# Kernel optimization log

Hardware: AMD Instinct MI355X
Metric: run time of the kernel (lower is better)

The kernel has to match this reference:

```python
import jax, jax.numpy as jnp
import numpy as np

THETA = 1.0
DILATIONS = (1, 2, 3, 4)
EPS = 1e-6


def _scale_features(x, d):
    # x: [B, C, H, W]; one pyramid scale (dilation d)
    B, C, H, W = x.shape
    k = 3 + 2 * (d - 1)          # kernel size per original formula
    pad = d * d                   # pad so effective span d*(k-1)+1 = 2d^2+1 preserves HxW
    K = k * k
    patches = jax.lax.conv_general_dilated_patches(
        x, (k, k), (1, 1), [(pad, pad), (pad, pad)], rhs_dilation=(d, d)
    )  # [B, C*K, H, W], channel-major per input channel
    p = patches.reshape(B, C, K, H, W)

    mu = p.mean(axis=2, keepdims=True)
    diff = p - mu
    var_biased = (diff * diff).mean(axis=2)                 # E[(p-mu)^2]
    std = jnp.sqrt(var_biased * (K / (K - 1))) + EPS        # torch .std is unbiased (ddof=1)

    contrast = var_biased / (std * std)                     # mean(normed^2)
    energy = (p * p).mean(axis=2)
    entropy = -(p * jnp.log(p + EPS)).mean(axis=2)
    # NB: original precedence -> 1.0 / mean(1 + |p - mu|)
    homogeneity = 1.0 / ((1.0 + jnp.abs(diff)).mean(axis=2))

    feats = jnp.stack([contrast, energy, entropy, homogeneity], axis=2)  # [B, C, 4, H, W]
    # martingale transform: exp(theta*log(f+eps) - 0.5*theta^2)
    M = jnp.exp(THETA * jnp.log(feats + EPS) - 0.5 * THETA ** 2)
    return M.reshape(B, C * 4, H, W)  # cat over channels of per-channel feature stacks


def setup_inputs() -> dict:
    key = jax.random.key(0)
    x = jax.random.uniform(key, (2, 4, 256, 256), dtype=jnp.float32)
    return {"x": x}


def reference(x):
    return tuple(_scale_features(x, d) for d in DILATIONS)
```

## Files before the change

### kernel.cpp

```cpp
#include <hip/hip_runtime.h>
#include <cstddef>

#define EPS 1e-6f
constexpr float INV_SQRT_E = 0.6065306597126334f;

template <int D>
__device__ __forceinline__ void body(const float* __restrict__ x,
                                     float* __restrict__ out,
                                     char* smem, int bc, int H, int W)
{
    constexpr int PAD = D * D;
    constexpr int KS  = 2 * D + 1;
    constexpr int K   = KS * KS;
    constexpr int TW  = 64, TH = 8;
    constexpr int LW  = TW + 2 * PAD;
    constexpr int LH  = TH + 2 * PAD;
    constexpr int NE  = LH * LW;
    constexpr int NI2 = (NE + 1023) / 1024;
    constexpr float INVK = 1.0f / (float)K;
    constexpr float UNB  = (float)K / (float)(K - 1);

    float*  sx  = (float*)smem;
    float*  slg = sx + NE;
    float2* cs2 = (float2*)(slg + NE);
    float*  cs1 = (float*)(cs2 + TH * LW);
    float*  muP  = (float*)cs2;
    float*  sadP = muP + TH * 64;

    const int w0 = blockIdx.x * TW;
    const int h0 = blockIdx.y * TH;
    const float* xp = x + (size_t)bc * H * W;
    const int tid = threadIdx.y * 64 + threadIdx.x;

    float v0b[NI2], v1b[NI2];
    #pragma unroll
    for (int i = 0; i < NI2; ++i) {
        const int e0 = 2 * (tid + i * 512);
        float v0 = 0.0f, v1 = 0.0f;
        if (e0 < NE) {
            const int r  = e0 / LW;
            const int cc = e0 - r * LW;
            const int gh = h0 - PAD + r;
            const int gw = w0 - PAD + cc;
            if (gh >= 0 && gh < H) {
                if constexpr ((PAD & 1) == 0) {
                    if (gw >= 0 && gw + 1 < W) {
                        const float2 v = *(const float2*)&xp[gh * W + gw];
                        v0 = v.x; v1 = v.y;
                    } else {
                        if (gw >= 0 && gw < W)         v0 = xp[gh * W + gw];
                        if (gw + 1 >= 0 && gw + 1 < W) v1 = xp[gh * W + gw + 1];
                    }
                } else {
                    if (gw >= 0 && gw < W)         v0 = xp[gh * W + gw];
                    if (gw + 1 >= 0 && gw + 1 < W) v1 = xp[gh * W + gw + 1];
                }
            }
        }
        v0b[i] = v0; v1b[i] = v1;
    }
    #pragma unroll
    for (int i = 0; i < NI2; ++i) {
        const int e0 = 2 * (tid + i * 512);
        if (e0 < NE) {
            *(float2*)&sx[e0]  = make_float2(v0b[i], v1b[i]);
            *(float2*)&slg[e0] = make_float2(v0b[i] * __logf(v0b[i] + EPS),
                                             v1b[i] * __logf(v1b[i] + EPS));
        }
    }
    __syncthreads();

    const int tx = threadIdx.x;
    const int ty = threadIdx.y;

    if constexpr (K <= 9) {
        const float* bx = sx  + ty * LW + tx;
        const float* bl = slg + ty * LW + tx;
        float s = 0.f, s2 = 0.f, sl = 0.f, ta[K];
        #pragma unroll
        for (int mi = 0; mi < KS; ++mi)
            #pragma unroll
            for (int mj = 0; mj < KS; ++mj) {
                const float v = bx[mi * LW + mj];
                ta[mi * KS + mj] = v;
                s  += v;
                s2  = fmaf(v, v, s2);
                sl += bl[mi * LW + mj];
            }
        const float mu = s * INVK;
        float sad = 0.f;
        #pragma unroll
        for (int i = 0; i < K; ++i) sad += fabsf(ta[i] - mu);

        const float energy   = s2 * INVK;
        const float var      = fmaxf(energy - mu * mu, 0.f);
        const float sd       = __builtin_amdgcn_sqrtf(var * UNB) + EPS;
        const float contrast = var * __builtin_amdgcn_rcpf(sd * sd);
        const float entropy  = -sl * INVK;
        const float homog    = __builtin_amdgcn_rcpf(fmaf(sad, INVK, 1.0f));
        const size_t fs = (size_t)H * W;
        const size_t ro = (size_t)(h0 + ty) * W;
        float* op = out + (size_t)bc * 4 * fs + w0 + tx;
        __builtin_nontemporal_store((contrast + EPS) * INV_SQRT_E, &op[0 * fs + ro]);
        __builtin_nontemporal_store((energy   + EPS) * INV_SQRT_E, &op[1 * fs + ro]);
        __builtin_nontemporal_store((entropy  + EPS) * INV_SQRT_E, &op[2 * fs + ro]);
        __builtin_nontemporal_store((homog    + EPS) * INV_SQRT_E, &op[3 * fs + ro]);
        return;
    } else {
        constexpr int HW2 = LW / 2;
        if (tid < 4 * HW2) {
            const int p  = tid / HW2;
            const int c2 = (tid - p * HW2) * 2;
            if (!(D == 3 && p == 3)) {
                const int vA = (D == 2) ? ((p < 2) ? p : p + 2) : p;
                const int vB = vA + D;
                const float2* cx = (const float2*)(sx + vA * LW + c2);
                float sA0=0,sA1=0,qA0=0,qA1=0,sB0=0,sB1=0,qB0=0,qB1=0;
                #pragma unroll
                for (int t = 0; t <= KS; ++t) {
                    const float2 v = cx[t * D * HW2];
                    if (t < KS) { sA0 += v.x; sA1 += v.y;
                                  qA0 = fmaf(v.x,v.x,qA0); qA1 = fmaf(v.y,v.y,qA1); }
                    if (t >= 1) { sB0 += v.x; sB1 += v.y;
                                  qB0 = fmaf(v.x,v.x,qB0); qB1 = fmaf(v.y,v.y,qB1); }
                }
                const float2* cl = (const float2*)(slg + vA * LW + c2);
                float lA0=0,lA1=0,lB0=0,lB1=0;
                #pragma unroll
                for (int t = 0; t <= KS; ++t) {
                    const float2 g = cl[t * D * HW2];
                    if (t < KS) { lA0 += g.x; lA1 += g.y; }
                    if (t >= 1) { lB0 += g.x; lB1 += g.y; }
                }
                *(float4*)&cs2[vA * LW + c2] = make_float4(sA0, qA0, sA1, qA1);
                *(float4*)&cs2[vB * LW + c2] = make_float4(sB0, qB0, sB1, qB1);
                *(float2*)&cs1[vA * LW + c2] = make_float2(lA0, lA1);
                *(float2*)&cs1[vB * LW + c2] = make_float2(lB0, lB1);
            } else {
                #pragma unroll
                for (int rr = 6; rr <= 7; ++rr) {
                    const float2* cx = (const float2*)(sx  + rr * LW + c2);
                    const float2* cl = (const float2*)(slg + rr * LW + c2);
                    float s0=0,s1=0,q0=0,q1=0,l0=0,l1=0;
                    #pragma unroll
                    for (int mi = 0; mi < KS; ++mi) {
                        const float2 v = cx[mi * D * HW2];
                        const float2 g = cl[mi * D * HW2];
                        s0 += v.x; s1 += v.y;
                        q0 = fmaf(v.x,v.x,q0); q1 = fmaf(v.y,v.y,q1);
                        l0 += g.x; l1 += g.y;
                    }
                    *(float4*)&cs2[rr * LW + c2] = make_float4(s0, q0, s1, q1);
                    *(float2*)&cs1[rr * LW + c2] = make_float2(l0, l1);
                }
            }
        }
        __syncthreads();

        float s = 0.f, s2 = 0.f, sl = 0.f;
        const float2* q2 = cs2 + ty * LW + tx;
        const float*  q1 = cs1 + ty * LW + tx;
        #pragma unroll
        for (int mj = 0; mj < KS; ++mj) {
            const float2 q = q2[mj * D];
            s += q.x; s2 += q.y; sl += q1[mj * D];
        }
        const float mu = s * INVK;
        __syncthreads();

        muP[ty * 64 + tx] = mu;
        __syncthreads();

        if (ty < 4) {
            const int o = ty;
            if (!(D == 3 && o == 3)) {
                const int rA = (D == 2) ? ((o < 2) ? o : o + 2) : o;
                const int rB = rA + D;
                const float muA = muP[rA * 64 + tx];
                const float muB = muP[rB * 64 + tx];
                float sadA = 0.f, sadB = 0.f;
                const float* bp = sx + rA * LW + tx;
                #pragma unroll
                for (int mj = 0; mj < KS; ++mj) {
                    const float* cp = bp + mj * D;
                    #pragma unroll
                    for (int t = 0; t <= KS; ++t) {
                        const float v = cp[t * D * LW];
                        if (t < KS) sadA += fabsf(v - muA);
                        if (t >= 1) sadB += fabsf(v - muB);
                    }
                }
                sadP[rA * 64 + tx] = sadA;
                sadP[rB * 64 + tx] = sadB;
            } else {
                #pragma unroll
                for (int rr = 6; rr <= 7; ++rr) {
                    const float mur = muP[rr * 64 + tx];
                    const float* bp = sx + rr * LW + tx;
                    float sd = 0.f;
                    #pragma unroll
                    for (int mi = 0; mi < KS; ++mi)
                        #pragma unroll
                        for (int mj = 0; mj < KS; ++mj)
                            sd += fabsf(bp[mi * D * LW + mj * D] - mur);
                    sadP[rr * 64 + tx] = sd;
                }
            }
        }
        __syncthreads();
        const float sad = sadP[ty * 64 + tx];

        const float energy   = s2 * INVK;
        const float var      = fmaxf(energy - mu * mu, 0.f);
        const float sd       = __builtin_amdgcn_sqrtf(var * UNB) + EPS;
        const float contrast = var * __builtin_amdgcn_rcpf(sd * sd);
        const float entropy  = -sl * INVK;
        const float homog    = __builtin_amdgcn_rcpf(fmaf(sad, INVK, 1.0f));
        const size_t fs = (size_t)H * W;
        const size_t ro = (size_t)(h0 + ty) * W;
        float* op = out + (size_t)bc * 4 * fs + w0 + tx;
        __builtin_nontemporal_store((contrast + EPS) * INV_SQRT_E, &op[0 * fs + ro]);
        __builtin_nontemporal_store((energy   + EPS) * INV_SQRT_E, &op[1 * fs + ro]);
        __builtin_nontemporal_store((entropy  + EPS) * INV_SQRT_E, &op[2 * fs + ro]);
        __builtin_nontemporal_store((homog    + EPS) * INV_SQRT_E, &op[3 * fs + ro]);
    }
}

__global__ __launch_bounds__(512, 8) void tex_fused(
    const float* __restrict__ x, float* __restrict__ out, int H, int W)
{
    extern __shared__ __align__(16) char smem[];
    const int dz = blockIdx.z & 3;
    const int bc = blockIdx.z >> 2;
    const size_t per = (size_t)8 * 4 * H * W;
    switch (dz) {
        case 0: body<4>(x, out + 3 * per, smem, bc, H, W); break;
        case 1: body<3>(x, out + 2 * per, smem, bc, H, W); break;
        case 2: body<2>(x, out + 1 * per, smem, bc, H, W); break;
        default: body<1>(x, out + 0 * per, smem, bc, H, W); break;
    }
}

extern "C" void kernel_launch(void* const* d_in, const int* in_sizes, int n_in,
                              void* d_out, int out_size, void* d_ws, size_t ws_size,
                              hipStream_t stream) {
    const float* x = (const float*)d_in[0];
    float* out = (float*)d_out;

    const int H = 256, W = 256;
    const size_t smem_bytes = 39936;

    dim3 blk(64, 8, 1);
    dim3 grd(W / 64, H / 8, 8 * 4);
    tex_fused<<<grd, blk, smem_bytes, stream>>>(x, out, H, W);
}
```

Measured before the change: 77.21 us.

## Double tile height to 16 rows and reuse vertical sums across row chains

Each block now covers 16 output rows instead of 8, so the halo overhead per output row shrinks. Vertical column sums and SAD are computed as chains that share loaded taps across several output rows spaced by the dilation. For D>1 the entropy log is computed on the fly, so the separate log tile is no longer stored and shared memory shrinks. The trade-off is that only a fraction of threads do the chain phases, which lowers parallelism, and the grid has half as many blocks.

```diff
diff --git a/kernel.cpp b/kernel.cpp
--- a/kernel.cpp
+++ b/kernel.cpp
@@ -3,6 +3,106 @@
 
 #define EPS 1e-6f
 constexpr float INV_SQRT_E = 0.6065306597126334f;
+
+
+template <int D, int J, int TAPS, int LW, int KS>
+__device__ __forceinline__ void vchain(const float* __restrict__ sx,
+                                       float* __restrict__ cs2f,
+                                       float* __restrict__ cs1,
+                                       const int r0, const int c2)
+{
+    constexpr int STEP2 = D * (LW / 2);
+    const float2* cx = (const float2*)(sx + r0 * LW + c2);
+    float s0[J], s1[J], q0[J], q1[J];
+#pragma unroll
+    for (int j = 0; j < J; ++j) { s0[j] = 0.f; s1[j] = 0.f; q0[j] = 0.f; q1[j] = 0.f; }
+#pragma unroll
+    for (int t = 0; t < TAPS; ++t) {
+        const float2 v = cx[t * STEP2];
+#pragma unroll
+        for (int j = 0; j < J; ++j)
+            if (t >= j && t < j + KS) {
+                s0[j] += v.x; s1[j] += v.y;
+                q0[j] = fmaf(v.x, v.x, q0[j]);
+                q1[j] = fmaf(v.y, v.y, q1[j]);
+            }
+    }
+#pragma unroll
+    for (int j = 0; j < J; ++j)
+        *(float4*)&cs2f[2 * ((r0 + D * j) * LW + c2)] =
+            make_float4(s0[j], q0[j], s1[j], q1[j]);
+    float l0[J], l1[J];
+#pragma unroll
+    for (int j = 0; j < J; ++j) { l0[j] = 0.f; l1[j] = 0.f; }
+#pragma unroll
+    for (int t = 0; t < TAPS; ++t) {
+        const float2 v = cx[t * STEP2];
+        const float g0 = v.x * __logf(v.x + EPS);
+        const float g1 = v.y * __logf(v.y + EPS);
+#pragma unroll
+        for (int j = 0; j < J; ++j)
+            if (t >= j && t < j + KS) { l0[j] += g0; l1[j] += g1; }
+    }
+#pragma unroll
+    for (int j = 0; j < J; ++j)
+        *(float2*)&cs1[(r0 + D * j) * LW + c2] = make_float2(l0[j], l1[j]);
+}
+
+template <int D, int J, int TAPS, int LW, int KS>
+__device__ __forceinline__ void sadchain_pair(const float* __restrict__ sx,
+                                              const float* __restrict__ muP,
+                                              float* __restrict__ sadP,
+                                              const int r0, const int c2)
+{
+    constexpr int STEP2 = D * (LW / 2);
+    float m0[J], m1[J], a0[J], a1[J];
+#pragma unroll
+    for (int j = 0; j < J; ++j) {
+        const float2 m = *(const float2*)&muP[(r0 + D * j) * 64 + c2];
+        m0[j] = m.x; m1[j] = m.y; a0[j] = 0.f; a1[j] = 0.f;
+    }
+#pragma unroll 1
+    for (int mj = 0; mj < KS; ++mj) {
+        const float2* cp = (const float2*)(sx + r0 * LW + c2 + D * mj);
+#pragma unroll
+        for (int t = 0; t < TAPS; ++t) {
+            const float2 v = cp[t * STEP2];
+#pragma unroll
+            for (int j = 0; j < J; ++j)
+                if (t >= j && t < j + KS) {
+                    a0[j] += fabsf(v.x - m0[j]);
+                    a1[j] += fabsf(v.y - m1[j]);
+                }
+        }
+    }
+#pragma unroll
+    for (int j = 0; j < J; ++j)
+        *(float2*)&sadP[(r0 + D * j) * 64 + c2] = make_float2(a0[j], a1[j]);
+}
+
+template <int D, int J, int TAPS, int LW, int KS>
+__device__ __forceinline__ void sadchain_scalar(const float* __restrict__ sx,
+                                                const float* __restrict__ muP,
+                                                float* __restrict__ sadP,
+                                                const int r0, const int c)
+{
+    float m[J], a[J];
+#pragma unroll
+    for (int j = 0; j < J; ++j) { m[j] = muP[(r0 + D * j) * 64 + c]; a[j] = 0.f; }
+#pragma unroll 1
+    for (int mj = 0; mj < KS; ++mj) {
+        const float* cp = sx + r0 * LW + c + D * mj;
+#pragma unroll
+        for (int t = 0; t < TAPS; ++t) {
+            const float v = cp[t * D * LW];
+#pragma unroll
+            for (int j = 0; j < J; ++j)
+                if (t >= j && t < j + KS) a[j] += fabsf(v - m[j]);
+        }
+    }
+#pragma unroll
+    for (int j = 0; j < J; ++j) sadP[(r0 + D * j) * 64 + c] = a[j];
+}
 
 template <int D>
 __device__ __forceinline__ void body(const float* __restrict__ x,
@@ -12,31 +112,33 @@
     constexpr int PAD = D * D;
     constexpr int KS  = 2 * D + 1;
     constexpr int K   = KS * KS;
-    constexpr int TW  = 64, TH = 8;
+    constexpr int TW  = 64, TH = 16;
     constexpr int LW  = TW + 2 * PAD;
     constexpr int LH  = TH + 2 * PAD;
     constexpr int NE  = LH * LW;
-    constexpr int NI2 = (NE + 1023) / 1024;
+    constexpr int NI2 = (NE / 2 + 511) / 512;
     constexpr float INVK = 1.0f / (float)K;
     constexpr float UNB  = (float)K / (float)(K - 1);
 
     float*  sx  = (float*)smem;
+    float2* cs2 = (float2*)(sx + NE);
+    float*  cs1 = (float*)(cs2 + 16 * LW);
+    float*  muP  = (float*)cs2;
+    float*  sadP = muP + 16 * 64;
     float*  slg = sx + NE;
-    float2* cs2 = (float2*)(slg + NE);
-    float*  cs1 = (float*)(cs2 + TH * LW);
-    float*  muP  = (float*)cs2;
-    float*  sadP = muP + TH * 64;
 
     const int w0 = blockIdx.x * TW;
     const int h0 = blockIdx.y * TH;
     const float* xp = x + (size_t)bc * H * W;
     const int tid = threadIdx.y * 64 + threadIdx.x;
+    const int tx = threadIdx.x;
+    const int ty = threadIdx.y;
 
     float v0b[NI2], v1b[NI2];
-    #pragma unroll
+#pragma unroll
     for (int i = 0; i < NI2; ++i) {
         const int e0 = 2 * (tid + i * 512);
-        float v0 = 0.0f, v1 = 0.0f;
+        float v0 = 0.f, v1 = 0.f;
         if (e0 < NE) {
             const int r  = e0 / LW;
             const int cc = e0 - r * LW;
@@ -59,170 +161,160 @@
         }
         v0b[i] = v0; v1b[i] = v1;
     }
-    #pragma unroll
+#pragma unroll
     for (int i = 0; i < NI2; ++i) {
         const int e0 = 2 * (tid + i * 512);
         if (e0 < NE) {
-            *(float2*)&sx[e0]  = make_float2(v0b[i], v1b[i]);
-            *(float2*)&slg[e0] = make_float2(v0b[i] * __logf(v0b[i] + EPS),
-                                             v1b[i] * __logf(v1b[i] + EPS));
+            *(float2*)&sx[e0] = make_float2(v0b[i], v1b[i]);
+            if constexpr (D == 1)
+                *(float2*)&slg[e0] = make_float2(v0b[i] * __logf(v0b[i] + EPS),
+                                                 v1b[i] * __logf(v1b[i] + EPS));
         }
     }
     __syncthreads();
 
-    const int tx = threadIdx.x;
-    const int ty = threadIdx.y;
+    const size_t fs = (size_t)H * W;
+    float* op = out + (size_t)bc * 4 * fs + w0 + tx;
 
     if constexpr (K <= 9) {
-        const float* bx = sx  + ty * LW + tx;
-        const float* bl = slg + ty * LW + tx;
-        float s = 0.f, s2 = 0.f, sl = 0.f, ta[K];
-        #pragma unroll
-        for (int mi = 0; mi < KS; ++mi)
-            #pragma unroll
-            for (int mj = 0; mj < KS; ++mj) {
-                const float v = bx[mi * LW + mj];
-                ta[mi * KS + mj] = v;
-                s  += v;
-                s2  = fmaf(v, v, s2);
-                sl += bl[mi * LW + mj];
-            }
-        const float mu = s * INVK;
-        float sad = 0.f;
-        #pragma unroll
-        for (int i = 0; i < K; ++i) sad += fabsf(ta[i] - mu);
-
-        const float energy   = s2 * INVK;
-        const float var      = fmaxf(energy - mu * mu, 0.f);
-        const float sd       = __builtin_amdgcn_sqrtf(var * UNB) + EPS;
-        const float contrast = var * __builtin_amdgcn_rcpf(sd * sd);
-        const float entropy  = -sl * INVK;
-        const float homog    = __builtin_amdgcn_rcpf(fmaf(sad, INVK, 1.0f));
-        const size_t fs = (size_t)H * W;
-        const size_t ro = (size_t)(h0 + ty) * W;
-        float* op = out + (size_t)bc * 4 * fs + w0 + tx;
-        __builtin_nontemporal_store((contrast + EPS) * INV_SQRT_E, &op[0 * fs + ro]);
-        __builtin_nontemporal_store((energy   + EPS) * INV_SQRT_E, &op[1 * fs + ro]);
-        __builtin_nontemporal_store((entropy  + EPS) * INV_SQRT_E, &op[2 * fs + ro]);
-        __builtin_nontemporal_store((homog    + EPS) * INV_SQRT_E, &op[3 * fs + ro]);
+        auto d1row = [&](int row) {
+            const float* bx = sx  + row * LW + tx;
+            const float* bl = slg + row * LW + tx;
+            float s = 0.f, s2 = 0.f, sl = 0.f, ta[9];
+#pragma unroll
+            for (int mi = 0; mi < 3; ++mi)
+#pragma unroll
+                for (int mj = 0; mj < 3; ++mj) {
+                    const float v = bx[mi * LW + mj];
+                    ta[mi * 3 + mj] = v;
+                    s += v; s2 = fmaf(v, v, s2);
+                    sl += bl[mi * LW + mj];
+                }
+            const float mu = s * INVK;
+            float sad = 0.f;
+#pragma unroll
+            for (int i = 0; i < 9; ++i) sad += fabsf(ta[i] - mu);
+            const float energy   = s2 * INVK;
+            const float var      = fmaxf(energy - mu * mu, 0.f);
+            const float sd       = __builtin_amdgcn_sqrtf(var * UNB) + EPS;
+            const float contrast = var * __builtin_amdgcn_rcpf(sd * sd);
+            const float entropy  = -sl * INVK;
+            const float homog    = __builtin_amdgcn_rcpf(fmaf(sad, INVK, 1.0f));
+            const size_t ro = (size_t)(h0 + row) * W;
+            __builtin_nontemporal_store((contrast + EPS) * INV_SQRT_E, &op[0 * fs + ro]);
+            __builtin_nontemporal_store((energy   + EPS) * INV_SQRT_E, &op[1 * fs + ro]);
+            __builtin_nontemporal_store((entropy  + EPS) * INV_SQRT_E, &op[2 * fs + ro]);
+            __builtin_nontemporal_store((homog    + EPS) * INV_SQRT_E, &op[3 * fs + ro]);
+        };
+        d1row(ty);
+        __builtin_amdgcn_sched_barrier(0);
+        d1row(ty + 8);
         return;
     } else {
-        constexpr int HW2 = LW / 2;
-        if (tid < 4 * HW2) {
-            const int p  = tid / HW2;
-            const int c2 = (tid - p * HW2) * 2;
-            if (!(D == 3 && p == 3)) {
-                const int vA = (D == 2) ? ((p < 2) ? p : p + 2) : p;
-                const int vB = vA + D;
-                const float2* cx = (const float2*)(sx + vA * LW + c2);
-                float sA0=0,sA1=0,qA0=0,qA1=0,sB0=0,sB1=0,qB0=0,qB1=0;
-                #pragma unroll
-                for (int t = 0; t <= KS; ++t) {
-                    const float2 v = cx[t * D * HW2];
-                    if (t < KS) { sA0 += v.x; sA1 += v.y;
-                                  qA0 = fmaf(v.x,v.x,qA0); qA1 = fmaf(v.y,v.y,qA1); }
-                    if (t >= 1) { sB0 += v.x; sB1 += v.y;
-                                  qB0 = fmaf(v.x,v.x,qB0); qB1 = fmaf(v.y,v.y,qB1); }
-                }
-                const float2* cl = (const float2*)(slg + vA * LW + c2);
-                float lA0=0,lA1=0,lB0=0,lB1=0;
-                #pragma unroll
-                for (int t = 0; t <= KS; ++t) {
-                    const float2 g = cl[t * D * HW2];
-                    if (t < KS) { lA0 += g.x; lA1 += g.y; }
-                    if (t >= 1) { lB0 += g.x; lB1 += g.y; }
-                }
-                *(float4*)&cs2[vA * LW + c2] = make_float4(sA0, qA0, sA1, qA1);
-                *(float4*)&cs2[vB * LW + c2] = make_float4(sB0, qB0, sB1, qB1);
-                *(float2*)&cs1[vA * LW + c2] = make_float2(lA0, lA1);
-                *(float2*)&cs1[vB * LW + c2] = make_float2(lB0, lB1);
-            } else {
-                #pragma unroll
-                for (int rr = 6; rr <= 7; ++rr) {
-                    const float2* cx = (const float2*)(sx  + rr * LW + c2);
-                    const float2* cl = (const float2*)(slg + rr * LW + c2);
-                    float s0=0,s1=0,q0=0,q1=0,l0=0,l1=0;
-                    #pragma unroll
-                    for (int mi = 0; mi < KS; ++mi) {
-                        const float2 v = cx[mi * D * HW2];
-                        const float2 g = cl[mi * D * HW2];
-                        s0 += v.x; s1 += v.y;
-                        q0 = fmaf(v.x,v.x,q0); q1 = fmaf(v.y,v.y,q1);
-                        l0 += g.x; l1 += g.y;
-                    }
-                    *(float4*)&cs2[rr * LW + c2] = make_float4(s0, q0, s1, q1);
-                    *(float2*)&cs1[rr * LW + c2] = make_float2(l0, l1);
-                }
+        if constexpr (D == 4) {
+            constexpr int NW = LW / 2;
+            if (tid < 4 * NW) {
+                const int p = tid / NW, c2 = (tid - p * NW) * 2;
+                vchain<4, 4, 12, LW, KS>(sx, (float*)cs2, cs1, p, c2);
+            }
+        } else if constexpr (D == 3) {
+            constexpr int NW = LW / 2;
+            if (tid < 3 * NW) {
+                const int p = tid / NW, c2 = (tid - p * NW) * 2;
+                if (p == 0) vchain<3, 6, 12, LW, KS>(sx, (float*)cs2, cs1, 0, c2);
+                else        vchain<3, 5, 11, LW, KS>(sx, (float*)cs2, cs1, p, c2);
+            }
+        } else {
+            constexpr int NW = LW / 2;
+            if (tid < 4 * NW) {
+                const int p = tid / NW, c2 = (tid - p * NW) * 2;
+                const int r0 = (p & 1) + ((p >> 1) << 3);
+                vchain<2, 4, 8, LW, KS>(sx, (float*)cs2, cs1, r0, c2);
             }
         }
         __syncthreads();
 
-        float s = 0.f, s2 = 0.f, sl = 0.f;
-        const float2* q2 = cs2 + ty * LW + tx;
-        const float*  q1 = cs1 + ty * LW + tx;
-        #pragma unroll
-        for (int mj = 0; mj < KS; ++mj) {
-            const float2 q = q2[mj * D];
-            s += q.x; s2 += q.y; sl += q1[mj * D];
-        }
-        const float mu = s * INVK;
+        float s2a, sla, mua, s2b, slb, mub;
+        {
+            const int row = ty;
+            float s = 0.f, s2 = 0.f, sl = 0.f;
+            const float2* q2 = cs2 + row * LW + tx;
+            const float*  q1 = cs1 + row * LW + tx;
+#pragma unroll
+            for (int mj = 0; mj < KS; ++mj) {
+                const float2 q = q2[mj * D];
+                s += q.x; s2 += q.y; sl += q1[mj * D];
+            }
+            s2a = s2; sla = sl; mua = s * INVK;
+        }
+        __builtin_amdgcn_sched_barrier(0);
+        {
+            const int row = ty + 8;
+            float s = 0.f, s2 = 0.f, sl = 0.f;
+            const float2* q2 = cs2 + row * LW + tx;
+            const float*  q1 = cs1 + row * LW + tx;
+#pragma unroll
+            for (int mj = 0; mj < KS; ++mj) {
+                const float2 q = q2[mj * D];
+                s += q.x; s2 += q.y; sl += q1[mj * D];
+            }
+            s2b = s2; slb = sl; mub = s * INVK;
+        }
         __syncthreads();
-
-        muP[ty * 64 + tx] = mu;
+        muP[ty * 64 + tx] = mua;
+        muP[(ty + 8) * 64 + tx] = mub;
         __syncthreads();
 
-        if (ty < 4) {
-            const int o = ty;
-            if (!(D == 3 && o == 3)) {
-                const int rA = (D == 2) ? ((o < 2) ? o : o + 2) : o;
-                const int rB = rA + D;
-                const float muA = muP[rA * 64 + tx];
-                const float muB = muP[rB * 64 + tx];
-                float sadA = 0.f, sadB = 0.f;
-                const float* bp = sx + rA * LW + tx;
-                #pragma unroll
-                for (int mj = 0; mj < KS; ++mj) {
-                    const float* cp = bp + mj * D;
-                    #pragma unroll
-                    for (int t = 0; t <= KS; ++t) {
-                        const float v = cp[t * D * LW];
-                        if (t < KS) sadA += fabsf(v - muA);
-                        if (t >= 1) sadB += fabsf(v - muB);
-                    }
-                }
-                sadP[rA * 64 + tx] = sadA;
-                sadP[rB * 64 + tx] = sadB;
-            } else {
-                #pragma unroll
-                for (int rr = 6; rr <= 7; ++rr) {
-                    const float mur = muP[rr * 64 + tx];
-                    const float* bp = sx + rr * LW + tx;
-                    float sd = 0.f;
-                    #pragma unroll
-                    for (int mi = 0; mi < KS; ++mi)
-                        #pragma unroll
-                        for (int mj = 0; mj < KS; ++mj)
-                            sd += fabsf(bp[mi * D * LW + mj * D] - mur);
-                    sadP[rr * 64 + tx] = sd;
-                }
+        if constexpr (D == 4) {
+            if (tid < 128) {
+                const int p = tid >> 5, c2 = (tid & 31) * 2;
+                sadchain_pair<4, 4, 12, LW, KS>(sx, muP, sadP, p, c2);
+            }
+        } else if constexpr (D == 2) {
+            if (tid < 128) {
+                const int p = tid >> 5, c2 = (tid & 31) * 2;
+                const int r0 = (p & 1) + ((p >> 1) << 3);
+                sadchain_pair<2, 4, 8, LW, KS>(sx, muP, sadP, r0, c2);
+            }
+        } else {
+            if (tid < 192) {
+                const int p = tid >> 6, c = tid & 63;
+                if (p == 0) sadchain_scalar<3, 6, 12, LW, KS>(sx, muP, sadP, 0, c);
+                else        sadchain_scalar<3, 5, 11, LW, KS>(sx, muP, sadP, p, c);
             }
         }
         __syncthreads();
-        const float sad = sadP[ty * 64 + tx];
-
-        const float energy   = s2 * INVK;
-        const float var      = fmaxf(energy - mu * mu, 0.f);
-        const float sd       = __builtin_amdgcn_sqrtf(var * UNB) + EPS;
-        const float contrast = var * __builtin_amdgcn_rcpf(sd * sd);
-        const float entropy  = -sl * INVK;
-        const float homog    = __builtin_amdgcn_rcpf(fmaf(sad, INVK, 1.0f));
-        const size_t fs = (size_t)H * W;
-        const size_t ro = (size_t)(h0 + ty) * W;
-        float* op = out + (size_t)bc * 4 * fs + w0 + tx;
-        __builtin_nontemporal_store((contrast + EPS) * INV_SQRT_E, &op[0 * fs + ro]);
-        __builtin_nontemporal_store((energy   + EPS) * INV_SQRT_E, &op[1 * fs + ro]);
-        __builtin_nontemporal_store((entropy  + EPS) * INV_SQRT_E, &op[2 * fs + ro]);
-        __builtin_nontemporal_store((homog    + EPS) * INV_SQRT_E, &op[3 * fs + ro]);
+
+        {
+            const int row = ty;
+            const float sad = sadP[row * 64 + tx];
+            const float energy   = s2a * INVK;
+            const float var      = fmaxf(energy - mua * mua, 0.f);
+            const float sd       = __builtin_amdgcn_sqrtf(var * UNB) + EPS;
+            const float contrast = var * __builtin_amdgcn_rcpf(sd * sd);
+            const float entropy  = -sla * INVK;
+            const float homog    = __builtin_amdgcn_rcpf(fmaf(sad, INVK, 1.0f));
+            const size_t ro = (size_t)(h0 + row) * W;
+            __builtin_nontemporal_store((contrast + EPS) * INV_SQRT_E, &op[0 * fs + ro]);
+            __builtin_nontemporal_store((energy   + EPS) * INV_SQRT_E, &op[1 * fs + ro]);
+            __builtin_nontemporal_store((entropy  + EPS) * INV_SQRT_E, &op[2 * fs + ro]);
+            __builtin_nontemporal_store((homog    + EPS) * INV_SQRT_E, &op[3 * fs + ro]);
+        }
+        {
+            const int row = ty + 8;
+            const float sad = sadP[row * 64 + tx];
+            const float energy   = s2b * INVK;
+            const float var      = fmaxf(energy - mub * mub, 0.f);
+            const float sd       = __builtin_amdgcn_sqrtf(var * UNB) + EPS;
+            const float contrast = var * __builtin_amdgcn_rcpf(sd * sd);
+            const float entropy  = -slb * INVK;
+            const float homog    = __builtin_amdgcn_rcpf(fmaf(sad, INVK, 1.0f));
+            const size_t ro = (size_t)(h0 + row) * W;
+            __builtin_nontemporal_store((contrast + EPS) * INV_SQRT_E, &op[0 * fs + ro]);
+            __builtin_nontemporal_store((energy   + EPS) * INV_SQRT_E, &op[1 * fs + ro]);
+            __builtin_nontemporal_store((entropy  + EPS) * INV_SQRT_E, &op[2 * fs + ro]);
+            __builtin_nontemporal_store((homog    + EPS) * INV_SQRT_E, &op[3 * fs + ro]);
+        }
     }
 }
 
@@ -248,9 +340,9 @@
     float* out = (float*)d_out;
 
     const int H = 256, W = 256;
-    const size_t smem_bytes = 39936;
+    const size_t smem_bytes = 36864;
 
     dim3 blk(64, 8, 1);
-    dim3 grd(W / 64, H / 8, 8 * 4);
+    dim3 grd(W / 64, H / 16, 8 * 4);
     tex_fused<<<grd, blk, smem_bytes, stream>>>(x, out, H, W);
 }
```

Measured after the change: 84.57 us. 9.5% more time.

## Split warps into SAD and stats groups to drop mean round-trip syncs

Applied to the files above, without the earlier changes.

Rows 0-3 of threads compute their own window means directly from the column sums and then the absolute-deviation sums. Rows 4-7 meanwhile compute the sum, squared-sum and log-sum statistics for two output rows each and write all outputs. This removes the shared-memory mean exchange and two barriers, letting the two kinds of work overlap across warps. The cost is that half the threads produce all stores, and the SAD buffer now reuses the log buffer region.

```diff
diff --git a/kernel.cpp b/kernel.cpp
--- a/kernel.cpp
+++ b/kernel.cpp
@@ -24,8 +24,7 @@
     float*  slg = sx + NE;
     float2* cs2 = (float2*)(slg + NE);
     float*  cs1 = (float*)(cs2 + TH * LW);
-    float*  muP  = (float*)cs2;
-    float*  sadP = muP + TH * 64;
+    float*  sadP = slg;
 
     const int w0 = blockIdx.x * TW;
     const int h0 = blockIdx.y * TH;
@@ -157,27 +156,22 @@
         }
         __syncthreads();
 
-        float s = 0.f, s2 = 0.f, sl = 0.f;
-        const float2* q2 = cs2 + ty * LW + tx;
-        const float*  q1 = cs1 + ty * LW + tx;
-        #pragma unroll
-        for (int mj = 0; mj < KS; ++mj) {
-            const float2 q = q2[mj * D];
-            s += q.x; s2 += q.y; sl += q1[mj * D];
-        }
-        const float mu = s * INVK;
-        __syncthreads();
-
-        muP[ty * 64 + tx] = mu;
-        __syncthreads();
-
+        float s2a, sla, mua, s2b, slb, mub;
         if (ty < 4) {
             const int o = ty;
             if (!(D == 3 && o == 3)) {
                 const int rA = (D == 2) ? ((o < 2) ? o : o + 2) : o;
                 const int rB = rA + D;
-                const float muA = muP[rA * 64 + tx];
-                const float muB = muP[rB * 64 + tx];
+                float sA = 0.f, sB = 0.f;
+                const float* cA = (const float*)(cs2 + rA * LW + tx);
+                const float* cB = (const float*)(cs2 + rB * LW + tx);
+                #pragma unroll
+                for (int mj = 0; mj < KS; ++mj) {
+                    sA += cA[2 * mj * D];
+                    sB += cB[2 * mj * D];
+                }
+                const float muA = sA * INVK;
+                const float muB = sB * INVK;
                 float sadA = 0.f, sadB = 0.f;
                 const float* bp = sx + rA * LW + tx;
                 #pragma unroll
@@ -195,7 +189,11 @@
             } else {
                 #pragma unroll
                 for (int rr = 6; rr <= 7; ++rr) {
-                    const float mur = muP[rr * 64 + tx];
+                    float sr = 0.f;
+                    const float* cR = (const float*)(cs2 + rr * LW + tx);
+                    #pragma unroll
+                    for (int mj = 0; mj < KS; ++mj) sr += cR[2 * mj * D];
+                    const float mur = sr * INVK;
                     const float* bp = sx + rr * LW + tx;
                     float sd = 0.f;
                     #pragma unroll
@@ -206,23 +204,66 @@
                     sadP[rr * 64 + tx] = sd;
                 }
             }
+        } else {
+            const int r0 = 2 * (ty - 4);
+            {
+                float s = 0.f, s2 = 0.f, sl = 0.f;
+                const float2* q2 = cs2 + r0 * LW + tx;
+                const float*  q1 = cs1 + r0 * LW + tx;
+                #pragma unroll
+                for (int mj = 0; mj < KS; ++mj) {
+                    const float2 q = q2[mj * D];
+                    s += q.x; s2 += q.y; sl += q1[mj * D];
+                }
+                s2a = s2; sla = sl; mua = s * INVK;
+            }
+            {
+                float s = 0.f, s2 = 0.f, sl = 0.f;
+                const float2* q2 = cs2 + (r0 + 1) * LW + tx;
+                const float*  q1 = cs1 + (r0 + 1) * LW + tx;
+                #pragma unroll
+                for (int mj = 0; mj < KS; ++mj) {
+                    const float2 q = q2[mj * D];
+                    s += q.x; s2 += q.y; sl += q1[mj * D];
+                }
+                s2b = s2; slb = sl; mub = s * INVK;
+            }
         }
         __syncthreads();
-        const float sad = sadP[ty * 64 + tx];
-
-        const float energy   = s2 * INVK;
-        const float var      = fmaxf(energy - mu * mu, 0.f);
-        const float sd       = __builtin_amdgcn_sqrtf(var * UNB) + EPS;
-        const float contrast = var * __builtin_amdgcn_rcpf(sd * sd);
-        const float entropy  = -sl * INVK;
-        const float homog    = __builtin_amdgcn_rcpf(fmaf(sad, INVK, 1.0f));
-        const size_t fs = (size_t)H * W;
-        const size_t ro = (size_t)(h0 + ty) * W;
-        float* op = out + (size_t)bc * 4 * fs + w0 + tx;
-        __builtin_nontemporal_store((contrast + EPS) * INV_SQRT_E, &op[0 * fs + ro]);
-        __builtin_nontemporal_store((energy   + EPS) * INV_SQRT_E, &op[1 * fs + ro]);
-        __builtin_nontemporal_store((entropy  + EPS) * INV_SQRT_E, &op[2 * fs + ro]);
-        __builtin_nontemporal_store((homog    + EPS) * INV_SQRT_E, &op[3 * fs + ro]);
+
+        if (ty >= 4) {
+            const int r0 = 2 * (ty - 4);
+            const size_t fs = (size_t)H * W;
+            float* op = out + (size_t)bc * 4 * fs + w0 + tx;
+            {
+                const float sad = sadP[r0 * 64 + tx];
+                const float energy   = s2a * INVK;
+                const float var      = fmaxf(energy - mua * mua, 0.f);
+                const float sd       = __builtin_amdgcn_sqrtf(var * UNB) + EPS;
+                const float contrast = var * __builtin_amdgcn_rcpf(sd * sd);
+                const float entropy  = -sla * INVK;
+                const float homog    = __builtin_amdgcn_rcpf(fmaf(sad, INVK, 1.0f));
+                const size_t ro = (size_t)(h0 + r0) * W;
+                __builtin_nontemporal_store((contrast + EPS) * INV_SQRT_E, &op[0 * fs + ro]);
+                __builtin_nontemporal_store((energy   + EPS) * INV_SQRT_E, &op[1 * fs + ro]);
+                __builtin_nontemporal_store((entropy  + EPS) * INV_SQRT_E, &op[2 * fs + ro]);
+                __builtin_nontemporal_store((homog    + EPS) * INV_SQRT_E, &op[3 * fs + ro]);
+            }
+            {
+                const float sad = sadP[(r0 + 1) * 64 + tx];
+                const float energy   = s2b * INVK;
+                const float var      = fmaxf(energy - mub * mub, 0.f);
+                const float sd       = __builtin_amdgcn_sqrtf(var * UNB) + EPS;
+                const float contrast = var * __builtin_amdgcn_rcpf(sd * sd);
+                const float entropy  = -slb * INVK;
+                const float homog    = __builtin_amdgcn_rcpf(fmaf(sad, INVK, 1.0f));
+                const size_t ro = (size_t)(h0 + r0 + 1) * W;
+                __builtin_nontemporal_store((contrast + EPS) * INV_SQRT_E, &op[0 * fs + ro]);
+                __builtin_nontemporal_store((energy   + EPS) * INV_SQRT_E, &op[1 * fs + ro]);
+                __builtin_nontemporal_store((entropy  + EPS) * INV_SQRT_E, &op[2 * fs + ro]);
+                __builtin_nontemporal_store((homog    + EPS) * INV_SQRT_E, &op[3 * fs + ro]);
+            }
+        }
     }
 }
 
```

Result: no change. 77.46 us (+0.3%).
